# Kernel optimization log

Measured on AMD Instinct MI355X. Metric: run time of the kernel, lower is better.

Reference implementation:

```python
import jax, jax.numpy as jnp
import numpy as np

N_ROWS = 4_194_304  # batch rows
N_LAYERS = 30


def setup_inputs() -> dict:
    key = jax.random.key(0)
    k1, k2, k3, k4, k5 = jax.random.split(key, 5)
    x1 = jax.random.normal(k1, (N_ROWS, 1), dtype=jnp.float32)
    x2 = jax.random.normal(k2, (N_ROWS, 5), dtype=jnp.float32)
    # Per-layer params stacked: Linear(5->1) weight [1,5] + bias [1]; Linear(1->5, no bias) weight [5,1]
    W1 = jax.random.normal(k3, (N_LAYERS, 1, 5), dtype=jnp.float32) * (1.0 / np.sqrt(5.0))
    b1 = jax.random.normal(k4, (N_LAYERS, 1), dtype=jnp.float32) * (1.0 / np.sqrt(5.0))
    W2 = jax.random.normal(k5, (N_LAYERS, 5, 1), dtype=jnp.float32)
    return {"x1": x1, "x2": x2, "W1": W1, "b1": b1, "W2": W2}


def reference(x1, x2, W1, b1, W2):
    # Chain of 30 UpDownDoubleResNetBlock blocks:
    #   x1 = x1 + relu(x2) @ W1^T + b1   (Linear(5,1) with bias)
    #   x2 = x2 + relu(x1) @ W2^T        (Linear(1,5) no bias)
    def step(carry, params):
        h1, h2 = carry
        w1, bb1, w2 = params  # [1,5], [1], [5,1]
        h1 = h1 + jax.nn.relu(h2) @ w1.T + bb1  # [N,1]
        h2 = h2 + jax.nn.relu(h1) @ w2.T        # [N,5]
        return (h1, h2), None

    (x1, x2), _ = jax.lax.scan(step, (x1, x2), (W1, b1, W2))
    return (x1, x2)
```

## Files before the change

### kernel.cpp

```cpp
#include <hip/hip_runtime.h>

#define NL 30

__global__ __launch_bounds__(256) void drn_kernel(
    const float* __restrict__ x1, const float* __restrict__ x2,
    const float* __restrict__ W1, const float* __restrict__ b1,
    const float* __restrict__ W2,
    float* __restrict__ o1, float* __restrict__ o2)
{
    __shared__ __align__(16) float sp[NL * 12];
    for (int i = threadIdx.x; i < NL * 12; i += 256) {
        int l = i / 12, k = i % 12;
        float v = 0.0f;
        if (k < 5)        v = W1[l * 5 + k];
        else if (k == 5)  v = b1[l];
        else if (k < 11)  v = W2[l * 5 + (k - 6)];
        sp[i] = v;
    }
    __syncthreads();

    int row = blockIdx.x * 256 + threadIdx.x;

    float h1 = x1[row];
    int b = row * 5;
    float h2[5];
    #pragma unroll
    for (int j = 0; j < 5; ++j) h2[j] = x2[b + j];

    for (int l = 0; l < NL; ++l) {
        float4 p0 = *(const float4*)&sp[l * 12];
        float4 p1 = *(const float4*)&sp[l * 12 + 4];
        float4 p2 = *(const float4*)&sp[l * 12 + 8];
        float s = h1 + p1.y;
        s = fmaf(fmaxf(h2[0], 0.f), p0.x, s);
        s = fmaf(fmaxf(h2[1], 0.f), p0.y, s);
        s = fmaf(fmaxf(h2[2], 0.f), p0.z, s);
        s = fmaf(fmaxf(h2[3], 0.f), p0.w, s);
        s = fmaf(fmaxf(h2[4], 0.f), p1.x, s);
        h1 = s;
        float rh = fmaxf(s, 0.f);
        h2[0] = fmaf(rh, p1.z, h2[0]);
        h2[1] = fmaf(rh, p1.w, h2[1]);
        h2[2] = fmaf(rh, p2.x, h2[2]);
        h2[3] = fmaf(rh, p2.y, h2[3]);
        h2[4] = fmaf(rh, p2.z, h2[4]);
    }

    o1[row] = h1;
    #pragma unroll
    for (int j = 0; j < 5; ++j) o2[b + j] = h2[j];
}

extern "C" void kernel_launch(void* const* d_in, const int* in_sizes, int n_in,
                              void* d_out, int out_size, void* d_ws, size_t ws_size,
                              hipStream_t stream) {
    const float* x1 = (const float*)d_in[0];
    const float* x2 = (const float*)d_in[1];
    const float* W1 = (const float*)d_in[2];
    const float* b1 = (const float*)d_in[3];
    const float* W2 = (const float*)d_in[4];
    int nrows = in_sizes[0];
    float* o1 = (float*)d_out;
    float* o2 = (float*)d_out + nrows;

    int block = 256;
    int grid = nrows / block;
    drn_kernel<<<grid, block, 0, stream>>>(x1, x2, W1, b1, W2, o1, o2);
}
```

Measured before the change: 191.9 us.

## Process four rows per thread with packed float2 FMAs and vectorized loads

Each thread now handles four rows, loading x1 and x2 with float4 vector accesses and computing pairs of rows with two-wide vector FMAs so the compiler can emit packed FP32 instructions. The layer loop is fully unrolled and weights are read directly from global memory as uniform scalars, which removes the shared-memory staging and the barrier. The grid shrinks fourfold. In exchange, register pressure rises, fewer threads are in flight to hide memory latency, and the per-thread x2 accesses are strided.

```diff
diff --git a/kernel.cpp b/kernel.cpp
--- a/kernel.cpp
+++ b/kernel.cpp
@@ -1,6 +1,16 @@
 #include <hip/hip_runtime.h>
 
 #define NL 30
+
+typedef float v2f __attribute__((ext_vector_type(2)));
+
+static __device__ __forceinline__ v2f vsplat(float x) { v2f r; r.x = x; r.y = x; return r; }
+static __device__ __forceinline__ v2f vrelu(v2f a) {
+    v2f r; r.x = fmaxf(a.x, 0.f); r.y = fmaxf(a.y, 0.f); return r;
+}
+static __device__ __forceinline__ v2f vfma(v2f a, v2f b, v2f c) {
+    return __builtin_elementwise_fma(a, b, c);
+}
 
 __global__ __launch_bounds__(256) void drn_kernel(
     const float* __restrict__ x1, const float* __restrict__ x2,
@@ -8,47 +18,66 @@
     const float* __restrict__ W2,
     float* __restrict__ o1, float* __restrict__ o2)
 {
-    __shared__ __align__(16) float sp[NL * 12];
-    for (int i = threadIdx.x; i < NL * 12; i += 256) {
-        int l = i / 12, k = i % 12;
-        float v = 0.0f;
-        if (k < 5)        v = W1[l * 5 + k];
-        else if (k == 5)  v = b1[l];
-        else if (k < 11)  v = W2[l * 5 + (k - 6)];
-        sp[i] = v;
-    }
-    __syncthreads();
+    const int tid = blockIdx.x * 256 + threadIdx.x;
 
-    int row = blockIdx.x * 256 + threadIdx.x;
+    const float4 a1 = ((const float4*)x1)[tid];
+    v2f h1a = {a1.x, a1.y};
+    v2f h1b = {a1.z, a1.w};
 
-    float h1 = x1[row];
-    int b = row * 5;
-    float h2[5];
+    const float4* x2v = (const float4*)x2 + tid * 5;
+    float4 q0 = x2v[0], q1 = x2v[1], q2 = x2v[2], q3 = x2v[3], q4 = x2v[4];
+    const float r[20] = {q0.x,q0.y,q0.z,q0.w, q1.x,q1.y,q1.z,q1.w,
+                         q2.x,q2.y,q2.z,q2.w, q3.x,q3.y,q3.z,q3.w,
+                         q4.x,q4.y,q4.z,q4.w};
+    v2f h2a[5], h2b[5];
     #pragma unroll
-    for (int j = 0; j < 5; ++j) h2[j] = x2[b + j];
-
-    for (int l = 0; l < NL; ++l) {
-        float4 p0 = *(const float4*)&sp[l * 12];
-        float4 p1 = *(const float4*)&sp[l * 12 + 4];
-        float4 p2 = *(const float4*)&sp[l * 12 + 8];
-        float s = h1 + p1.y;
-        s = fmaf(fmaxf(h2[0], 0.f), p0.x, s);
-        s = fmaf(fmaxf(h2[1], 0.f), p0.y, s);
-        s = fmaf(fmaxf(h2[2], 0.f), p0.z, s);
-        s = fmaf(fmaxf(h2[3], 0.f), p0.w, s);
-        s = fmaf(fmaxf(h2[4], 0.f), p1.x, s);
-        h1 = s;
-        float rh = fmaxf(s, 0.f);
-        h2[0] = fmaf(rh, p1.z, h2[0]);
-        h2[1] = fmaf(rh, p1.w, h2[1]);
-        h2[2] = fmaf(rh, p2.x, h2[2]);
-        h2[3] = fmaf(rh, p2.y, h2[3]);
-        h2[4] = fmaf(rh, p2.z, h2[4]);
+    for (int j = 0; j < 5; ++j) {
+        h2a[j].x = r[j];      h2a[j].y = r[5 + j];
+        h2b[j].x = r[10 + j]; h2b[j].y = r[15 + j];
     }
 
-    o1[row] = h1;
     #pragma unroll
-    for (int j = 0; j < 5; ++j) o2[b + j] = h2[j];
+    for (int l = 0; l < NL; ++l) {
+        const v2f vw1[5] = {vsplat(W1[l*5+0]), vsplat(W1[l*5+1]), vsplat(W1[l*5+2]),
+                            vsplat(W1[l*5+3]), vsplat(W1[l*5+4])};
+        const v2f vbb  = vsplat(b1[l]);
+        const v2f vw2[5] = {vsplat(W2[l*5+0]), vsplat(W2[l*5+1]), vsplat(W2[l*5+2]),
+                            vsplat(W2[l*5+3]), vsplat(W2[l*5+4])};
+
+        {
+            v2f s = h1a + vbb;
+            #pragma unroll
+            for (int j = 0; j < 5; ++j) s = vfma(vrelu(h2a[j]), vw1[j], s);
+            h1a = s;
+            const v2f rh = vrelu(s);
+            #pragma unroll
+            for (int j = 0; j < 5; ++j) h2a[j] = vfma(rh, vw2[j], h2a[j]);
+        }
+        {
+            v2f s = h1b + vbb;
+            #pragma unroll
+            for (int j = 0; j < 5; ++j) s = vfma(vrelu(h2b[j]), vw1[j], s);
+            h1b = s;
+            const v2f rh = vrelu(s);
+            #pragma unroll
+            for (int j = 0; j < 5; ++j) h2b[j] = vfma(rh, vw2[j], h2b[j]);
+        }
+    }
+
+    ((float4*)o1)[tid] = make_float4(h1a.x, h1a.y, h1b.x, h1b.y);
+
+    float w[20];
+    #pragma unroll
+    for (int j = 0; j < 5; ++j) {
+        w[j]      = h2a[j].x;  w[5 + j]  = h2a[j].y;
+        w[10 + j] = h2b[j].x;  w[15 + j] = h2b[j].y;
+    }
+    float4* o2v = (float4*)o2 + tid * 5;
+    o2v[0] = make_float4(w[0],  w[1],  w[2],  w[3]);
+    o2v[1] = make_float4(w[4],  w[5],  w[6],  w[7]);
+    o2v[2] = make_float4(w[8],  w[9],  w[10], w[11]);
+    o2v[3] = make_float4(w[12], w[13], w[14], w[15]);
+    o2v[4] = make_float4(w[16], w[17], w[18], w[19]);
 }
 
 extern "C" void kernel_launch(void* const* d_in, const int* in_sizes, int n_in,
@@ -64,6 +93,6 @@
     float* o2 = (float*)d_out + nrows;
 
     int block = 256;
-    int grid = nrows / block;
+    int grid = nrows / (block * 4);
     drn_kernel<<<grid, block, 0, stream>>>(x1, x2, W1, b1, W2, o1, o2);
 }
```

Result: slower. 198.0 us (+3.2%).

## Stage x2 through LDS, process two rows per thread with packed FMA

Applied to the files above, without the earlier changes.

Each block now handles 512 rows, with two rows per thread. The 5-wide x2 rows are loaded and stored coalesced through an LDS slab instead of strided per-thread accesses. Parameters are duplicated into pairs so packed v2 FMA instructions can compute both rows at once. The layer loop is fully unrolled and outputs use nontemporal stores. This adds LDS traffic, extra syncs and register pressure, and halves the grid size.

```diff
diff --git a/kernel.cpp b/kernel.cpp
--- a/kernel.cpp
+++ b/kernel.cpp
@@ -1,6 +1,19 @@
 #include <hip/hip_runtime.h>
 
 #define NL 30
+#define RPB 512
+
+typedef float v2f __attribute__((ext_vector_type(2)));
+typedef float v4f __attribute__((ext_vector_type(4)));
+
+static __device__ __forceinline__ v2f flo(v4f v) { v2f r; r.x = v.x; r.y = v.y; return r; }
+static __device__ __forceinline__ v2f fhi(v4f v) { v2f r; r.x = v.z; r.y = v.w; return r; }
+static __device__ __forceinline__ v2f vrelu(v2f a) {
+    v2f r; r.x = fmaxf(a.x, 0.f); r.y = fmaxf(a.y, 0.f); return r;
+}
+static __device__ __forceinline__ v2f vfma(v2f a, v2f b, v2f c) {
+    return __builtin_elementwise_fma(a, b, c);
+}
 
 __global__ __launch_bounds__(256) void drn_kernel(
     const float* __restrict__ x1, const float* __restrict__ x2,
@@ -8,47 +21,82 @@
     const float* __restrict__ W2,
     float* __restrict__ o1, float* __restrict__ o2)
 {
-    __shared__ __align__(16) float sp[NL * 12];
-    for (int i = threadIdx.x; i < NL * 12; i += 256) {
-        int l = i / 12, k = i % 12;
+    __shared__ __align__(16) float sp[NL * 24];
+    __shared__ __align__(16) float slab[RPB * 5];
+
+    for (int i = threadIdx.x; i < NL * 24; i += 256) {
+        int p = i >> 1, l = p / 12, k = p % 12;
         float v = 0.0f;
         if (k < 5)        v = W1[l * 5 + k];
         else if (k == 5)  v = b1[l];
         else if (k < 11)  v = W2[l * 5 + (k - 6)];
         sp[i] = v;
     }
+
+    const int t = threadIdx.x;
+    const int base = blockIdx.x * RPB;
+
+    v2f h1;
+    h1.x = x1[base + t];
+    h1.y = x1[base + 256 + t];
+
+    const v2f* g2 = (const v2f*)(x2 + (size_t)base * 5);
+    v2f* s2 = (v2f*)slab;
+    #pragma unroll
+    for (int k = 0; k < 5; ++k)
+        s2[t + 256 * k] = g2[t + 256 * k];
     __syncthreads();
 
-    int row = blockIdx.x * 256 + threadIdx.x;
-
-    float h1 = x1[row];
-    int b = row * 5;
-    float h2[5];
+    v2f h2[5];
     #pragma unroll
-    for (int j = 0; j < 5; ++j) h2[j] = x2[b + j];
-
-    for (int l = 0; l < NL; ++l) {
-        float4 p0 = *(const float4*)&sp[l * 12];
-        float4 p1 = *(const float4*)&sp[l * 12 + 4];
-        float4 p2 = *(const float4*)&sp[l * 12 + 8];
-        float s = h1 + p1.y;
-        s = fmaf(fmaxf(h2[0], 0.f), p0.x, s);
-        s = fmaf(fmaxf(h2[1], 0.f), p0.y, s);
-        s = fmaf(fmaxf(h2[2], 0.f), p0.z, s);
-        s = fmaf(fmaxf(h2[3], 0.f), p0.w, s);
-        s = fmaf(fmaxf(h2[4], 0.f), p1.x, s);
-        h1 = s;
-        float rh = fmaxf(s, 0.f);
-        h2[0] = fmaf(rh, p1.z, h2[0]);
-        h2[1] = fmaf(rh, p1.w, h2[1]);
-        h2[2] = fmaf(rh, p2.x, h2[2]);
-        h2[3] = fmaf(rh, p2.y, h2[3]);
-        h2[4] = fmaf(rh, p2.z, h2[4]);
+    for (int j = 0; j < 5; ++j) {
+        h2[j].x = slab[5 * t + j];
+        h2[j].y = slab[5 * t + 1280 + j];
     }
 
-    o1[row] = h1;
+    const v4f* spv = (const v4f*)sp;
     #pragma unroll
-    for (int j = 0; j < 5; ++j) o2[b + j] = h2[j];
+    for (int l = 0; l < NL; ++l) {
+        const v4f L0 = spv[l * 6 + 0];
+        const v4f L1 = spv[l * 6 + 1];
+        const v4f L2 = spv[l * 6 + 2];
+        const v4f L3 = spv[l * 6 + 3];
+        const v4f L4 = spv[l * 6 + 4];
+        const v4f L5 = spv[l * 6 + 5];
+        const v2f w10 = flo(L0), w11 = fhi(L0), w12 = flo(L1), w13 = fhi(L1),
+                  w14 = flo(L2), vbb = fhi(L2),
+                  w20 = flo(L3), w21 = fhi(L3), w22 = flo(L4), w23 = fhi(L4),
+                  w24 = flo(L5);
+
+        v2f s = h1 + vbb;
+        s = vfma(vrelu(h2[0]), w10, s);
+        s = vfma(vrelu(h2[1]), w11, s);
+        s = vfma(vrelu(h2[2]), w12, s);
+        s = vfma(vrelu(h2[3]), w13, s);
+        s = vfma(vrelu(h2[4]), w14, s);
+        h1 = s;
+        const v2f rh = vrelu(s);
+        h2[0] = vfma(rh, w20, h2[0]);
+        h2[1] = vfma(rh, w21, h2[1]);
+        h2[2] = vfma(rh, w22, h2[2]);
+        h2[3] = vfma(rh, w23, h2[3]);
+        h2[4] = vfma(rh, w24, h2[4]);
+    }
+
+    __builtin_nontemporal_store(h1.x, &o1[base + t]);
+    __builtin_nontemporal_store(h1.y, &o1[base + 256 + t]);
+
+    __syncthreads();
+    #pragma unroll
+    for (int j = 0; j < 5; ++j) {
+        slab[5 * t + j]        = h2[j].x;
+        slab[5 * t + 1280 + j] = h2[j].y;
+    }
+    __syncthreads();
+    v2f* go2 = (v2f*)(o2 + (size_t)base * 5);
+    #pragma unroll
+    for (int k = 0; k < 5; ++k)
+        __builtin_nontemporal_store(s2[t + 256 * k], &go2[t + 256 * k]);
 }
 
 extern "C" void kernel_launch(void* const* d_in, const int* in_sizes, int n_in,
@@ -64,6 +112,6 @@
     float* o2 = (float*)d_out + nrows;
 
     int block = 256;
-    int grid = nrows / block;
+    int grid = nrows / RPB;
     drn_kernel<<<grid, block, 0, stream>>>(x1, x2, W1, b1, W2, o1, o2);
 }
```

After: 195.6 us. No clear change (+1.9%).

## Stage x2 through LDS with vector loads, process four rows per thread

Applied to the files above, without the earlier changes.

Each block now handles 1024 rows. The 5-wide x2 rows are staged through shared memory with coalesced 16-byte loads and stores, replacing strided per-thread scalar accesses. Layer parameters are read from global memory with a one-layer-ahead prefetch instead of a shared table, and the layer loop is fully unrolled over four independent rows per thread to add ILP. Outputs use nontemporal stores. In exchange it uses 20KB of LDS per block and more registers, which may limit occupancy, and it assumes nrows is divisible by 1024.

```diff
diff --git a/kernel.cpp b/kernel.cpp
--- a/kernel.cpp
+++ b/kernel.cpp
@@ -1,54 +1,90 @@
 #include <hip/hip_runtime.h>
 
 #define NL 30
+#define RPT 4
+#define RPB (256 * RPT)
 
-__global__ __launch_bounds__(256) void drn_kernel(
+typedef float v2f __attribute__((ext_vector_type(2)));
+typedef float v4f __attribute__((ext_vector_type(4)));
+
+__global__ __launch_bounds__(256, 8) void drn_kernel(
     const float* __restrict__ x1, const float* __restrict__ x2,
     const float* __restrict__ W1, const float* __restrict__ b1,
     const float* __restrict__ W2,
     float* __restrict__ o1, float* __restrict__ o2)
 {
-    __shared__ __align__(16) float sp[NL * 12];
-    for (int i = threadIdx.x; i < NL * 12; i += 256) {
-        int l = i / 12, k = i % 12;
-        float v = 0.0f;
-        if (k < 5)        v = W1[l * 5 + k];
-        else if (k == 5)  v = b1[l];
-        else if (k < 11)  v = W2[l * 5 + (k - 6)];
-        sp[i] = v;
-    }
+    __shared__ __align__(16) float slab[RPB * 5];
+
+    const int t = threadIdx.x;
+    const int base = blockIdx.x * RPB;
+
+    const v4f* g2 = (const v4f*)(x2 + (size_t)base * 5);
+    v4f* s4 = (v4f*)slab;
+    #pragma unroll
+    for (int k = 0; k < 5; ++k)
+        s4[t + 256 * k] = g2[t + 256 * k];
+
+    float h1[RPT];
+    #pragma unroll
+    for (int r = 0; r < RPT; ++r) h1[r] = x1[base + 256 * r + t];
+
     __syncthreads();
 
-    int row = blockIdx.x * 256 + threadIdx.x;
+    float h2[RPT][5];
+    #pragma unroll
+    for (int r = 0; r < RPT; ++r)
+        #pragma unroll
+        for (int j = 0; j < 5; ++j)
+            h2[r][j] = slab[5 * (256 * r + t) + j];
 
-    float h1 = x1[row];
-    int b = row * 5;
-    float h2[5];
+    float pw10 = W1[0], pw11 = W1[1], pw12 = W1[2], pw13 = W1[3], pw14 = W1[4];
+    float pbb  = b1[0];
+    float pw20 = W2[0], pw21 = W2[1], pw22 = W2[2], pw23 = W2[3], pw24 = W2[4];
+
     #pragma unroll
-    for (int j = 0; j < 5; ++j) h2[j] = x2[b + j];
-
     for (int l = 0; l < NL; ++l) {
-        float4 p0 = *(const float4*)&sp[l * 12];
-        float4 p1 = *(const float4*)&sp[l * 12 + 4];
-        float4 p2 = *(const float4*)&sp[l * 12 + 8];
-        float s = h1 + p1.y;
-        s = fmaf(fmaxf(h2[0], 0.f), p0.x, s);
-        s = fmaf(fmaxf(h2[1], 0.f), p0.y, s);
-        s = fmaf(fmaxf(h2[2], 0.f), p0.z, s);
-        s = fmaf(fmaxf(h2[3], 0.f), p0.w, s);
-        s = fmaf(fmaxf(h2[4], 0.f), p1.x, s);
-        h1 = s;
-        float rh = fmaxf(s, 0.f);
-        h2[0] = fmaf(rh, p1.z, h2[0]);
-        h2[1] = fmaf(rh, p1.w, h2[1]);
-        h2[2] = fmaf(rh, p2.x, h2[2]);
-        h2[3] = fmaf(rh, p2.y, h2[3]);
-        h2[4] = fmaf(rh, p2.z, h2[4]);
+        const float w10 = pw10, w11 = pw11, w12 = pw12, w13 = pw13, w14 = pw14;
+        const float bb  = pbb;
+        const float w20 = pw20, w21 = pw21, w22 = pw22, w23 = pw23, w24 = pw24;
+        if (l + 1 < NL) {
+            const int n = (l + 1) * 5;
+            pw10 = W1[n+0]; pw11 = W1[n+1]; pw12 = W1[n+2]; pw13 = W1[n+3]; pw14 = W1[n+4];
+            pbb  = b1[l+1];
+            pw20 = W2[n+0]; pw21 = W2[n+1]; pw22 = W2[n+2]; pw23 = W2[n+3]; pw24 = W2[n+4];
+        }
+        #pragma unroll
+        for (int r = 0; r < RPT; ++r) {
+            float s = h1[r] + bb;
+            s = fmaf(fmaxf(h2[r][0], 0.f), w10, s);
+            s = fmaf(fmaxf(h2[r][1], 0.f), w11, s);
+            s = fmaf(fmaxf(h2[r][2], 0.f), w12, s);
+            s = fmaf(fmaxf(h2[r][3], 0.f), w13, s);
+            s = fmaf(fmaxf(h2[r][4], 0.f), w14, s);
+            h1[r] = s;
+            const float rh = fmaxf(s, 0.f);
+            h2[r][0] = fmaf(rh, w20, h2[r][0]);
+            h2[r][1] = fmaf(rh, w21, h2[r][1]);
+            h2[r][2] = fmaf(rh, w22, h2[r][2]);
+            h2[r][3] = fmaf(rh, w23, h2[r][3]);
+            h2[r][4] = fmaf(rh, w24, h2[r][4]);
+        }
     }
 
-    o1[row] = h1;
     #pragma unroll
-    for (int j = 0; j < 5; ++j) o2[b + j] = h2[j];
+    for (int r = 0; r < RPT; ++r)
+        __builtin_nontemporal_store(h1[r], &o1[base + 256 * r + t]);
+
+    __syncthreads();
+    #pragma unroll
+    for (int r = 0; r < RPT; ++r)
+        #pragma unroll
+        for (int j = 0; j < 5; ++j)
+            slab[5 * (256 * r + t) + j] = h2[r][j];
+    __syncthreads();
+    v4f* go2 = (v4f*)(o2 + (size_t)base * 5);
+    #pragma unroll
+    for (int k = 0; k < 5; ++k)
+        __builtin_nontemporal_store(s4[t + 256 * k], &go2[t + 256 * k]);
 }
 
 extern "C" void kernel_launch(void* const* d_in, const int* in_sizes, int n_in,
@@ -64,6 +100,6 @@
     float* o2 = (float*)d_out + nrows;
 
     int block = 256;
-    int grid = nrows / block;
+    int grid = nrows / RPB;
     drn_kernel<<<grid, block, 0, stream>>>(x1, x2, W1, b1, W2, o1, o2);
 }
```

Measured after the change: 194.5 us. No clear change (+1.3%).
